# Kernel optimization log

Hardware: AMD Instinct MI355X
Metric: run time of the kernel (lower is better)

## Reference

```python
import jax, jax.numpy as jnp
import numpy as np

H, T, E = 8, 2048, 512


def setup_inputs() -> dict:
    key = jax.random.key(0)
    ks = jax.random.split(key, 11)
    s_e = 1.0 / np.sqrt(E)
    s_f = 1.0 / np.sqrt(H * T)
    return {
        "x": jax.random.normal(ks[0], (T, E), jnp.float32),
        "y": jax.random.normal(ks[1], (T, E), jnp.float32),
        "z": jax.random.normal(ks[2], (T, E), jnp.float32),
        "Wq": jax.random.normal(ks[3], (H, E, E), jnp.float32) * s_e,
        "bq": jax.random.normal(ks[4], (H, E), jnp.float32) * s_e,
        "Wk": jax.random.normal(ks[5], (H, E, E), jnp.float32) * s_e,
        "bk": jax.random.normal(ks[6], (H, E), jnp.float32) * s_e,
        "Wv": jax.random.normal(ks[7], (H, E, E), jnp.float32) * s_e,
        "bv": jax.random.normal(ks[8], (H, E), jnp.float32) * s_e,
        "Wf": jax.random.normal(ks[9], (T, H * T), jnp.float32) * s_f,
        "bf": jax.random.normal(ks[10], (T,), jnp.float32) * s_f,
    }


def reference(x, y, z, Wq, bq, Wk, bk, Wv, bv, Wf, bf):
    # Per-head projections: torch Linear is x @ W.T + b, W is [out,in]
    q = jnp.einsum("se,hfe->hsf", x, Wq) + bq[:, None, :]  # [H,T,E]
    k = jnp.einsum("se,hfe->hsf", y, Wk) + bk[:, None, :]
    v = jnp.einsum("se,hfe->hsf", z, Wv) + bv[:, None, :]
    # Scores scaled by sqrt(num query rows) = sqrt(T), as in the source
    scores = jnp.einsum("hsf,htf->hst", q, k) / jnp.sqrt(jnp.asarray(T, x.dtype))
    att = jax.nn.softmax(scores, axis=-1)
    heads_out = jnp.einsum("hst,htf->hsf", att, v)  # [H,T,E]
    concat = heads_out.reshape(H * T, E)  # cat along dim 0
    # finalLinear applied to concat.T: [E, H*T] @ Wf.T -> [E, T], then transpose
    final = (concat.T @ Wf.T + bf).T  # [T, E]
    residual = final + z
    # Manual per-row LayerNorm: (x - mean) / sqrt(std^2 + 1e-4), population std
    mean = jnp.mean(residual, axis=1, keepdims=True)
    var = jnp.var(residual, axis=1, keepdims=True)
    return (residual - mean) / jnp.sqrt(var + 1e-4)
```

## Files before the change

kernel.cpp:

```cpp
#include <hip/hip_runtime.h>
#include <hip/hip_bf16.h>
#include <cstdint>


#define HH 8
#define TT 2048
#define EE 512
#define HT (HH * TT)
#define HE (HH * EE)

typedef __bf16 bf16_t;
typedef __attribute__((ext_vector_type(8))) __bf16 bf16x8;
typedef __attribute__((ext_vector_type(4))) float f32x4;

__device__ __forceinline__ void gld_lds16(const bf16_t* __restrict__ g, bf16_t* l) {
  __builtin_amdgcn_global_load_lds(
      (const __attribute__((address_space(1))) unsigned int*)g,
      (__attribute__((address_space(3))) unsigned int*)l, 16, 0, 0);
}

__device__ __forceinline__ bf16x8 cvt8(float4 u, float4 v) {
  bf16x8 o;
  o[0] = (__bf16)u.x; o[1] = (__bf16)u.y; o[2] = (__bf16)u.z; o[3] = (__bf16)u.w;
  o[4] = (__bf16)v.x; o[5] = (__bf16)v.y; o[6] = (__bf16)v.z; o[7] = (__bf16)v.w;
  return o;
}

template <typename AT, typename CT>
__global__ __launch_bounds__(512, 4) void mfma_gemm_nt(
    const AT* __restrict__ A, const bf16_t* __restrict__ B, CT* __restrict__ C,
    const float* __restrict__ bias_m, const float* __restrict__ bias_n,
    int K, int lda, int ldb, int ldc,
    int64_t sA, int64_t sB, int64_t sC, int64_t sBM, int64_t sBN) {
  const int gx = gridDim.x, gy = gridDim.y;
  const int nwg = gx * gy * (int)gridDim.z;
  const int lin = blockIdx.x + gx * (blockIdx.y + gy * blockIdx.z);
  const int qn = nwg >> 3, rn = nwg & 7;
  const int xcd = lin & 7, sub = lin >> 3;
  const int wgid = (xcd < rn ? xcd * (qn + 1) : rn * (qn + 1) + (xcd - rn) * qn) + sub;
  const int bx = wgid % gx;
  const int t1 = wgid / gx;
  const int by = t1 % gy;
  const int z = t1 / gy;

  A += z * sA;
  B += z * sB;
  C += z * sC;
  if (bias_m) bias_m += z * sBM;
  if (bias_n) bias_n += z * sBN;

  const int m0 = bx * 128;
  const int n0 = by * 128;
  const int tid = threadIdx.x;

  __shared__ bf16_t sAb[2][128 * 64];
  __shared__ bf16_t sBb[2][128 * 64];

  const int srow = tid >> 3;
  const int sc = tid & 7;
  const int csw = (sc ^ (srow & 7)) * 8;
  const AT* a0 = A + (int64_t)(m0 + srow) * lda + csw;
  const AT* a1 = a0 + (int64_t)64 * lda;
  const bf16_t* b0 = B + (int64_t)(n0 + srow) * ldb + csw;
  const bf16_t* b1 = b0 + (int64_t)64 * ldb;

  const int wave = tid >> 6;
  const int lane = tid & 63;
  const int wm = (wave >> 2) * 64;
  const int wn = (wave & 3) * 32;
  const int fr = lane & 15;
  const int qd = lane >> 4;
  const int cx0 = ((0 * 4 + qd) ^ (fr & 7)) * 8;
  const int cx1 = ((1 * 4 + qd) ^ (fr & 7)) * 8;

  f32x4 acc[4][2];
#pragma unroll
  for (int i = 0; i < 4; i++)
#pragma unroll
    for (int j = 0; j < 2; j++) acc[i][j] = (f32x4){0.f, 0.f, 0.f, 0.f};

  float4 pa[4];

#define STAGE_B(buf, kt)                                   \
  do {                                                     \
    gld_lds16(b0 + (kt), &sBb[buf][tid * 8]);              \
    gld_lds16(b1 + (kt), &sBb[buf][4096 + tid * 8]);       \
  } while (0)

#define STAGE_A_BF16(buf, kt)                              \
  do {                                                     \
    gld_lds16(a0 + (kt), &sAb[buf][tid * 8]);              \
    gld_lds16(a1 + (kt), &sAb[buf][4096 + tid * 8]);       \
  } while (0)

#define LOAD_A_F32(kt)                                     \
  do {                                                     \
    pa[0] = ((const float4*)(a0 + (kt)))[0];               \
    pa[1] = ((const float4*)(a0 + (kt)))[1];               \
    pa[2] = ((const float4*)(a1 + (kt)))[0];               \
    pa[3] = ((const float4*)(a1 + (kt)))[1];               \
  } while (0)

#define WRITE_A_F32(buf)                                      \
  do {                                                        \
    *(bf16x8*)&sAb[buf][tid * 8] = cvt8(pa[0], pa[1]);        \
    *(bf16x8*)&sAb[buf][4096 + tid * 8] = cvt8(pa[2], pa[3]); \
  } while (0)

#define COMPUTE(buf)                                                                    \
  do {                                                                                  \
    bf16x8 af[2][4], bfr[2][2];                                                         \
    _Pragma("unroll") for (int i = 0; i < 4; i++) {                                     \
      const int ar = (wm + i * 16 + fr) * 64;                                           \
      af[0][i] = *(const bf16x8*)&sAb[buf][ar + cx0];                                   \
      af[1][i] = *(const bf16x8*)&sAb[buf][ar + cx1];                                   \
    }                                                                                   \
    _Pragma("unroll") for (int j = 0; j < 2; j++) {                                     \
      const int br = (wn + j * 16 + fr) * 64;                                           \
      bfr[0][j] = *(const bf16x8*)&sBb[buf][br + cx0];                                  \
      bfr[1][j] = *(const bf16x8*)&sBb[buf][br + cx1];                                  \
    }                                                                                   \
    _Pragma("unroll") for (int ks = 0; ks < 2; ks++)                                    \
        _Pragma("unroll") for (int i = 0; i < 4; i++)                                   \
            _Pragma("unroll") for (int j = 0; j < 2; j++)                               \
                acc[i][j] = __builtin_amdgcn_mfma_f32_16x16x32_bf16(                    \
                    af[ks][i], bfr[ks][j], acc[i][j], 0, 0, 0);                         \
  } while (0)

  if constexpr (sizeof(AT) == 2) {
    STAGE_A_BF16(0, 0);
  } else {
    LOAD_A_F32(0);
    WRITE_A_F32(0);
  }
  STAGE_B(0, 0);
  __syncthreads();

  for (int kt = 0; kt < K; kt += 128) {
    if constexpr (sizeof(AT) == 2) {
      STAGE_A_BF16(1, kt + 64);
    } else {
      LOAD_A_F32(kt + 64);
    }
    STAGE_B(1, kt + 64);
    COMPUTE(0);
    if constexpr (sizeof(AT) == 4) WRITE_A_F32(1);
    __syncthreads();

    const bool more = (kt + 128) < K;
    if (more) {
      if constexpr (sizeof(AT) == 2) {
        STAGE_A_BF16(0, kt + 128);
      } else {
        LOAD_A_F32(kt + 128);
      }
      STAGE_B(0, kt + 128);
    }
    COMPUTE(1);
    if constexpr (sizeof(AT) == 4) {
      if (more) WRITE_A_F32(0);
    }
    __syncthreads();
  }

#undef STAGE_B
#undef STAGE_A_BF16
#undef LOAD_A_F32
#undef WRITE_A_F32
#undef COMPUTE

#pragma unroll
  for (int i = 0; i < 4; i++) {
    const int row0 = m0 + wm + i * 16 + qd * 4;
#pragma unroll
    for (int j = 0; j < 2; j++) {
      const int col = n0 + wn + j * 16 + fr;
      const float bn = bias_n ? bias_n[col] : 0.f;
#pragma unroll
      for (int r = 0; r < 4; r++) {
        const float bm = bias_m ? bias_m[row0 + r] : 0.f;
        C[(int64_t)(row0 + r) * ldc + col] = (CT)(acc[i][j][r] + bn + bm);
      }
    }
  }
}

__global__ __launch_bounds__(256) void cvt_bf16(const float* __restrict__ s,
                                                bf16_t* __restrict__ d) {
  const int64_t i = ((int64_t)blockIdx.x * 256 + threadIdx.x) * 8;
  float4 u = ((const float4*)(s + i))[0];
  float4 v = ((const float4*)(s + i))[1];
  *(bf16x8*)(d + i) = cvt8(u, v);
}

__global__ __launch_bounds__(256) void softmax_rows(bf16_t* __restrict__ S) {
  const float scale = 0.022097086912079608f;
  bf16_t* p = S + (int64_t)blockIdx.x * TT;
  const int tid = threadIdx.x;
  bf16x8 in = *(const bf16x8*)(p + tid * 8);
  float v[8];
  float mx = -1e30f;
#pragma unroll
  for (int i = 0; i < 8; i++) {
    v[i] = (float)in[i] * scale;
    mx = fmaxf(mx, v[i]);
  }
#pragma unroll
  for (int o = 32; o > 0; o >>= 1) mx = fmaxf(mx, __shfl_xor(mx, o));
  __shared__ float redm[4], reds[4];
  if ((tid & 63) == 0) redm[tid >> 6] = mx;
  __syncthreads();
  mx = fmaxf(fmaxf(redm[0], redm[1]), fmaxf(redm[2], redm[3]));
  float sum = 0.f;
#pragma unroll
  for (int i = 0; i < 8; i++) {
    v[i] = __expf(v[i] - mx);
    sum += v[i];
  }
#pragma unroll
  for (int o = 32; o > 0; o >>= 1) sum += __shfl_xor(sum, o);
  if ((tid & 63) == 0) reds[tid >> 6] = sum;
  __syncthreads();
  sum = reds[0] + reds[1] + reds[2] + reds[3];
  const float inv = 1.0f / sum;
  bf16x8 o8;
#pragma unroll
  for (int i = 0; i < 8; i++) o8[i] = (__bf16)(v[i] * inv);
  *(bf16x8*)(p + tid * 8) = o8;
}

__global__ __launch_bounds__(256) void ln_res(const float* __restrict__ F,
                                              const float* __restrict__ Z,
                                              const float* __restrict__ BF,
                                              float* __restrict__ O, int np) {
  const int row = blockIdx.x;
  const int tid = threadIdx.x;
  const int64_t off = (int64_t)row * EE + tid;
  float a = 0.f, b = 0.f;
  for (int pz = 0; pz < np; pz++) {
    const float* f = F + (int64_t)pz * TT * EE;
    a += f[off];
    b += f[off + 256];
  }
  const float bft = BF[row];
  a += bft + Z[off];
  b += bft + Z[off + 256];
  float s = a + b, ss = a * a + b * b;
#pragma unroll
  for (int w = 32; w > 0; w >>= 1) {
    s += __shfl_xor(s, w);
    ss += __shfl_xor(ss, w);
  }
  __shared__ float rs[4], rss[4];
  if ((tid & 63) == 0) {
    rs[tid >> 6] = s;
    rss[tid >> 6] = ss;
  }
  __syncthreads();
  s = rs[0] + rs[1] + rs[2] + rs[3];
  ss = rss[0] + rss[1] + rss[2] + rss[3];
  const float mean = s * (1.0f / EE);
  const float var = ss * (1.0f / EE) - mean * mean;
  const float inv = rsqrtf(var + 1e-4f);
  float* o = O + (int64_t)row * EE;
  o[tid] = (a - mean) * inv;
  o[tid + 256] = (b - mean) * inv;
}

extern "C" void kernel_launch(void* const* d_in, const int* in_sizes, int n_in,
                              void* d_out, int out_size, void* d_ws, size_t ws_size,
                              hipStream_t stream) {
  const float* x = (const float*)d_in[0];
  const float* y = (const float*)d_in[1];
  const float* z = (const float*)d_in[2];
  const float* Wq = (const float*)d_in[3];
  const float* bq = (const float*)d_in[4];
  const float* Wk = (const float*)d_in[5];
  const float* bk = (const float*)d_in[6];
  const float* Wv = (const float*)d_in[7];
  const float* bv = (const float*)d_in[8];
  const float* Wf = (const float*)d_in[9];
  const float* bfb = (const float*)d_in[10];
  float* out = (float*)d_out;

  const size_t MB = 1ull << 20;
  char* p = (char*)d_ws;

  const int64_t nTE = (int64_t)TT * EE;
  const int64_t nW = (int64_t)HH * EE * EE;

  if (ws_size >= 151 * MB) {
    bf16_t* xb = (bf16_t*)(p + 0 * MB);
    bf16_t* yb = (bf16_t*)(p + 2 * MB);
    bf16_t* zb = (bf16_t*)(p + 4 * MB);
    bf16_t* Wqb = (bf16_t*)(p + 6 * MB);
    bf16_t* Wkb = (bf16_t*)(p + 10 * MB);
    bf16_t* Wvb = (bf16_t*)(p + 14 * MB);
    bf16_t* q = (bf16_t*)(p + 18 * MB);
    bf16_t* k = (bf16_t*)(p + 34 * MB);
    bf16_t* vT = (bf16_t*)(p + 50 * MB);
    bf16_t* att = (bf16_t*)(p + 66 * MB);
    bf16_t* hoT = (bf16_t*)(p + 130 * MB);
    float* finp = (float*)(p + 66 * MB);

    cvt_bf16<<<nTE / 2048, 256, 0, stream>>>(x, xb);
    cvt_bf16<<<nTE / 2048, 256, 0, stream>>>(y, yb);
    cvt_bf16<<<nTE / 2048, 256, 0, stream>>>(z, zb);
    cvt_bf16<<<nW / 2048, 256, 0, stream>>>(Wq, Wqb);
    cvt_bf16<<<nW / 2048, 256, 0, stream>>>(Wk, Wkb);
    cvt_bf16<<<nW / 2048, 256, 0, stream>>>(Wv, Wvb);

    mfma_gemm_nt<bf16_t, bf16_t><<<dim3(16, 32, 1), 512, 0, stream>>>(
        xb, Wqb, q, nullptr, bq, EE, EE, EE, HE, 0, 0, 0, 0, 0);
    mfma_gemm_nt<bf16_t, bf16_t><<<dim3(16, 32, 1), 512, 0, stream>>>(
        yb, Wkb, k, nullptr, bk, EE, EE, EE, HE, 0, 0, 0, 0, 0);
    mfma_gemm_nt<bf16_t, bf16_t><<<dim3(32, 16, 1), 512, 0, stream>>>(
        Wvb, zb, vT, bv, nullptr, EE, EE, EE, TT, 0, 0, 0, 0, 0);
    mfma_gemm_nt<bf16_t, bf16_t><<<dim3(16, 16, 8), 512, 0, stream>>>(
        q, k, att, nullptr, nullptr, EE, HE, HE, TT, EE, EE, (int64_t)TT * TT, 0, 0);
    softmax_rows<<<HH * TT, 256, 0, stream>>>(att);
    mfma_gemm_nt<bf16_t, bf16_t><<<dim3(4, 16, 8), 512, 0, stream>>>(
        vT, att, hoT, nullptr, nullptr, TT, TT, TT, HT, (int64_t)EE * TT, (int64_t)TT * TT,
        (int64_t)TT, 0, 0);
    mfma_gemm_nt<float, float><<<dim3(16, 4, 8), 512, 0, stream>>>(
        Wf, hoT, finp, nullptr, nullptr, HT / 8, HT, HT, EE, HT / 8, HT / 8,
        (int64_t)TT * EE, 0, 0);
    ln_res<<<TT, 256, 0, stream>>>(finp, z, bfb, out, 8);
  } else {
    bf16_t* xb = (bf16_t*)(p + 0 * MB);
    bf16_t* yb = (bf16_t*)(p + 2 * MB);
    bf16_t* zb = (bf16_t*)(p + 4 * MB);
    bf16_t* Wqb = (bf16_t*)(p + 6 * MB);
    bf16_t* Wkb = (bf16_t*)(p + 10 * MB);
    bf16_t* Wvb = (bf16_t*)(p + 14 * MB);
    bf16_t* qh = (bf16_t*)(p + 18 * MB);
    bf16_t* kh = (bf16_t*)(p + 20 * MB);
    bf16_t* vTh = (bf16_t*)(p + 22 * MB);
    bf16_t* att = (bf16_t*)(p + 24 * MB);
    bf16_t* hoT = (bf16_t*)(p + 32 * MB);
    float* finp = (float*)(p + 0 * MB);

    cvt_bf16<<<nTE / 2048, 256, 0, stream>>>(x, xb);
    cvt_bf16<<<nTE / 2048, 256, 0, stream>>>(y, yb);
    cvt_bf16<<<nTE / 2048, 256, 0, stream>>>(z, zb);
    cvt_bf16<<<nW / 2048, 256, 0, stream>>>(Wq, Wqb);
    cvt_bf16<<<nW / 2048, 256, 0, stream>>>(Wk, Wkb);
    cvt_bf16<<<nW / 2048, 256, 0, stream>>>(Wv, Wvb);

    for (int h = 0; h < HH; h++) {
      const bf16_t* Wq_h = Wqb + (int64_t)h * EE * EE;
      const bf16_t* Wk_h = Wkb + (int64_t)h * EE * EE;
      const bf16_t* Wv_h = Wvb + (int64_t)h * EE * EE;
      mfma_gemm_nt<bf16_t, bf16_t><<<dim3(16, 4, 1), 512, 0, stream>>>(
          xb, Wq_h, qh, nullptr, bq + h * EE, EE, EE, EE, EE, 0, 0, 0, 0, 0);
      mfma_gemm_nt<bf16_t, bf16_t><<<dim3(16, 4, 1), 512, 0, stream>>>(
          yb, Wk_h, kh, nullptr, bk + h * EE, EE, EE, EE, EE, 0, 0, 0, 0, 0);
      mfma_gemm_nt<bf16_t, bf16_t><<<dim3(4, 16, 1), 512, 0, stream>>>(
          Wv_h, zb, vTh, bv + h * EE, nullptr, EE, EE, EE, TT, 0, 0, 0, 0, 0);
      mfma_gemm_nt<bf16_t, bf16_t><<<dim3(16, 16, 1), 512, 0, stream>>>(
          qh, kh, att, nullptr, nullptr, EE, EE, EE, TT, 0, 0, 0, 0, 0);
      softmax_rows<<<TT, 256, 0, stream>>>(att);
      mfma_gemm_nt<bf16_t, bf16_t><<<dim3(4, 16, 1), 512, 0, stream>>>(
          vTh, att, hoT + (int64_t)h * TT, nullptr, nullptr, TT, TT, TT, HT, 0, 0, 0, 0, 0);
    }
    mfma_gemm_nt<float, float><<<dim3(16, 4, 8), 512, 0, stream>>>(
        Wf, hoT, finp, nullptr, nullptr, HT / 8, HT, HT, EE, HT / 8, HT / 8,
        (int64_t)TT * EE, 0, 0);
    ln_res<<<TT, 256, 0, stream>>>(finp, z, bfb, out, 8);
  }
}
```

Baseline: 430.5 us.

## Add 256x256-tile 8-phase pipelined bf16 GEMM for QK projections and scores

Adds a new GEMM kernel with 256x256 output tiles per 512-thread block and 128KB of LDS. Its software pipeline interleaves direct global-to-LDS loads, LDS fragment reads and MFMA quadrants with explicit waitcnt, barriers and setprio. It is used for the attention score GEMM, and for the Q and K projections, which are merged into one batched launch by relying on the contiguous workspace layout plus a device copy of the two bias vectors. Larger tiles raise data reuse per LDS load and cut launch count, but the grids become much smaller (256 and 512 blocks) and the kernel can hold fewer waves per CU.

```diff
diff --git a/kernel.cpp b/kernel.cpp
--- a/kernel.cpp
+++ b/kernel.cpp
@@ -24,6 +24,171 @@
   o[0] = (__bf16)u.x; o[1] = (__bf16)u.y; o[2] = (__bf16)u.z; o[3] = (__bf16)u.w;
   o[4] = (__bf16)v.x; o[5] = (__bf16)v.y; o[6] = (__bf16)v.z; o[7] = (__bf16)v.w;
   return o;
+}
+
+#define XCD_SWIZZLE()                                                              \
+  const int gx = gridDim.x, gy = gridDim.y;                                        \
+  const int nwg = gx * gy * (int)gridDim.z;                                        \
+  const int lin = blockIdx.x + gx * (blockIdx.y + gy * blockIdx.z);                \
+  const int qn_ = nwg >> 3, rn_ = nwg & 7;                                         \
+  const int xcd_ = lin & 7, sub_ = lin >> 3;                                       \
+  const int wgid =                                                                 \
+      (xcd_ < rn_ ? xcd_ * (qn_ + 1) : rn_ * (qn_ + 1) + (xcd_ - rn_) * qn_) + sub_; \
+  const int bx = wgid % gx;                                                        \
+  const int t1_ = wgid / gx;                                                       \
+  const int by = t1_ % gy;                                                         \
+  const int z = t1_ / gy;
+
+template <typename CT>
+__global__ __launch_bounds__(512, 2) void gemm256_8ph(
+    const bf16_t* __restrict__ A, const bf16_t* __restrict__ B, CT* __restrict__ C,
+    const float* __restrict__ bias_n,
+    int K, int lda, int ldb, int ldc,
+    int64_t sA, int64_t sB, int64_t sC, int64_t sBN) {
+  XCD_SWIZZLE();
+  A += z * sA;
+  B += z * sB;
+  C += z * sC;
+  if (bias_n) bias_n += z * sBN;
+
+  const int m0 = bx * 256;
+  const int n0 = by * 256;
+  const int tid = threadIdx.x;
+
+  __shared__ bf16_t lds[65536];
+  bf16_t* sAl = lds;
+  bf16_t* sBl = lds + 32768;
+
+  const int srow = tid >> 3;
+  const int csw = ((tid & 7) ^ (srow & 7)) * 8;
+  const bf16_t* aS = A + (int64_t)(m0 + srow) * lda + csw;
+  const bf16_t* bS = B + (int64_t)(n0 + srow) * ldb + csw;
+  const int64_t l64a = (int64_t)64 * lda, l64b = (int64_t)64 * ldb;
+
+  const int wave = tid >> 6, lane = tid & 63;
+  const int wr = wave >> 2, wc = wave & 3;
+  const int fr = lane & 15, qd = lane >> 4;
+  const int aoff = wr * 8192 + fr * 64;
+  const int boff = wc * 4096 + fr * 64;
+  const int ck0 = ((0 * 4 + qd) ^ (fr & 7)) * 8;
+  const int ck1 = ((1 * 4 + qd) ^ (fr & 7)) * 8;
+
+  f32x4 acc[8][4];
+#pragma unroll
+  for (int i = 0; i < 8; i++)
+#pragma unroll
+    for (int j = 0; j < 4; j++) acc[i][j] = (f32x4){0.f, 0.f, 0.f, 0.f};
+
+  bf16x8 aR[2][8];
+  bf16x8 bR[2][2];
+
+#define STG_A(d, h, t)                                                        \
+  do {                                                                        \
+    const bf16_t* g_ = aS + (int64_t)(h) * 128 * lda + (int64_t)(t) * 64;     \
+    gld_lds16(g_, &sAl[(d) * 16384 + (h) * 8192 + tid * 8]);                  \
+    gld_lds16(g_ + l64a, &sAl[(d) * 16384 + (h) * 8192 + 4096 + tid * 8]);    \
+  } while (0)
+#define STG_B(d, h, t)                                                        \
+  do {                                                                        \
+    const bf16_t* g_ = bS + (int64_t)(h) * 128 * ldb + (int64_t)(t) * 64;     \
+    gld_lds16(g_, &sBl[(d) * 16384 + (h) * 8192 + tid * 8]);                  \
+    gld_lds16(g_ + l64b, &sBl[(d) * 16384 + (h) * 8192 + 4096 + tid * 8]);    \
+  } while (0)
+#define RD_A(d, ih)                                                           \
+  _Pragma("unroll") for (int i_ = 0; i_ < 4; i_++) {                          \
+    const int b_ = (d) * 16384 + aoff + ((ih) * 4 + i_) * 1024;               \
+    aR[0][(ih) * 4 + i_] = *(const bf16x8*)&sAl[b_ + ck0];                    \
+    aR[1][(ih) * 4 + i_] = *(const bf16x8*)&sAl[b_ + ck1];                    \
+  }
+#define RD_B(d, jh)                                                           \
+  _Pragma("unroll") for (int j_ = 0; j_ < 2; j_++) {                          \
+    const int b_ = (d) * 16384 + boff + ((jh) * 2 + j_) * 1024;               \
+    bR[0][j_] = *(const bf16x8*)&sBl[b_ + ck0];                               \
+    bR[1][j_] = *(const bf16x8*)&sBl[b_ + ck1];                               \
+  }
+#define MM(qm, qn)                                                            \
+  do {                                                                        \
+    __builtin_amdgcn_s_setprio(1);                                            \
+    _Pragma("unroll") for (int ks = 0; ks < 2; ks++)                          \
+        _Pragma("unroll") for (int i_ = 0; i_ < 4; i_++)                      \
+            _Pragma("unroll") for (int j_ = 0; j_ < 2; j_++)                  \
+                acc[(qm) * 4 + i_][(qn) * 2 + j_] =                           \
+                    __builtin_amdgcn_mfma_f32_16x16x32_bf16(                  \
+                        aR[ks][(qm) * 4 + i_], bR[ks][j_],                    \
+                        acc[(qm) * 4 + i_][(qn) * 2 + j_], 0, 0, 0);          \
+    __builtin_amdgcn_s_setprio(0);                                            \
+  } while (0)
+#define BAR __builtin_amdgcn_s_barrier()
+#define LGKM0                                                                 \
+  do {                                                                        \
+    asm volatile("s_waitcnt lgkmcnt(0)" ::: "memory");                        \
+    __builtin_amdgcn_sched_barrier(0);                                        \
+  } while (0)
+#define VMC(n)                                                                \
+  do {                                                                        \
+    asm volatile("s_waitcnt vmcnt(" #n ")" ::: "memory");                     \
+    __builtin_amdgcn_sched_barrier(0);                                        \
+  } while (0)
+
+  const int NT = K >> 6;
+
+  STG_A(0, 0, 0); STG_A(0, 1, 0); STG_B(0, 0, 0); STG_B(0, 1, 0);
+  STG_A(1, 0, 1); STG_A(1, 1, 1);
+  VMC(4);
+  BAR;
+
+  for (int t0 = 0; t0 < NT; t0 += 2) {
+    const int t1 = t0 + 1;
+    const bool m2 = (t0 + 2) < NT;
+    RD_A(0, 0); RD_B(0, 0);
+    STG_B(1, 0, t1);
+    BAR; LGKM0; MM(0, 0); BAR;
+    RD_A(0, 1);
+    STG_B(1, 1, t1);
+    BAR; LGKM0; MM(1, 0); BAR;
+    RD_B(0, 1);
+    if (m2) STG_A(0, 0, t0 + 2);
+    BAR; LGKM0; MM(0, 1); BAR;
+    if (m2) STG_A(0, 1, t0 + 2);
+    BAR; MM(1, 1);
+    if (m2) { VMC(4); } else { VMC(0); }
+    BAR;
+    RD_A(1, 0); RD_B(1, 0);
+    if (m2) STG_B(0, 0, t0 + 2);
+    BAR; LGKM0; MM(0, 0); BAR;
+    RD_A(1, 1);
+    if (m2) STG_B(0, 1, t0 + 2);
+    BAR; LGKM0; MM(1, 0); BAR;
+    RD_B(1, 1);
+    if (m2) STG_A(1, 0, t1 + 2);
+    BAR; LGKM0; MM(0, 1); BAR;
+    if (m2) STG_A(1, 1, t1 + 2);
+    BAR; MM(1, 1);
+    if (m2) VMC(4);
+    BAR;
+  }
+
+#undef STG_A
+#undef STG_B
+#undef RD_A
+#undef RD_B
+#undef MM
+#undef BAR
+#undef LGKM0
+#undef VMC
+
+#pragma unroll
+  for (int i = 0; i < 8; i++) {
+    const int row0 = m0 + wr * 128 + i * 16 + qd * 4;
+#pragma unroll
+    for (int j = 0; j < 4; j++) {
+      const int col = n0 + wc * 64 + j * 16 + fr;
+      const float bn = bias_n ? bias_n[col] : 0.f;
+#pragma unroll
+      for (int r = 0; r < 4; r++)
+        C[(int64_t)(row0 + r) * ldc + col] = (CT)(acc[i][j][r] + bn);
+    }
+  }
 }
 
 template <typename AT, typename CT>
@@ -32,17 +197,7 @@
     const float* __restrict__ bias_m, const float* __restrict__ bias_n,
     int K, int lda, int ldb, int ldc,
     int64_t sA, int64_t sB, int64_t sC, int64_t sBM, int64_t sBN) {
-  const int gx = gridDim.x, gy = gridDim.y;
-  const int nwg = gx * gy * (int)gridDim.z;
-  const int lin = blockIdx.x + gx * (blockIdx.y + gy * blockIdx.z);
-  const int qn = nwg >> 3, rn = nwg & 7;
-  const int xcd = lin & 7, sub = lin >> 3;
-  const int wgid = (xcd < rn ? xcd * (qn + 1) : rn * (qn + 1) + (xcd - rn) * qn) + sub;
-  const int bx = wgid % gx;
-  const int t1 = wgid / gx;
-  const int by = t1 % gy;
-  const int z = t1 / gy;
-
+  XCD_SWIZZLE();
   A += z * sA;
   B += z * sB;
   C += z * sC;
@@ -81,50 +236,46 @@
 
   float4 pa[4];
 
-#define STAGE_B(buf, kt)                                   \
-  do {                                                     \
-    gld_lds16(b0 + (kt), &sBb[buf][tid * 8]);              \
-    gld_lds16(b1 + (kt), &sBb[buf][4096 + tid * 8]);       \
-  } while (0)
-
-#define STAGE_A_BF16(buf, kt)                              \
-  do {                                                     \
-    gld_lds16(a0 + (kt), &sAb[buf][tid * 8]);              \
-    gld_lds16(a1 + (kt), &sAb[buf][4096 + tid * 8]);       \
-  } while (0)
-
-#define LOAD_A_F32(kt)                                     \
-  do {                                                     \
-    pa[0] = ((const float4*)(a0 + (kt)))[0];               \
-    pa[1] = ((const float4*)(a0 + (kt)))[1];               \
-    pa[2] = ((const float4*)(a1 + (kt)))[0];               \
-    pa[3] = ((const float4*)(a1 + (kt)))[1];               \
-  } while (0)
-
+#define STAGE_B(buf, kt)                              \
+  do {                                                \
+    gld_lds16(b0 + (kt), &sBb[buf][tid * 8]);         \
+    gld_lds16(b1 + (kt), &sBb[buf][4096 + tid * 8]);  \
+  } while (0)
+#define STAGE_A_BF16(buf, kt)                         \
+  do {                                                \
+    gld_lds16(a0 + (kt), &sAb[buf][tid * 8]);         \
+    gld_lds16(a1 + (kt), &sAb[buf][4096 + tid * 8]);  \
+  } while (0)
+#define LOAD_A_F32(kt)                                \
+  do {                                                \
+    pa[0] = ((const float4*)(a0 + (kt)))[0];          \
+    pa[1] = ((const float4*)(a0 + (kt)))[1];          \
+    pa[2] = ((const float4*)(a1 + (kt)))[0];          \
+    pa[3] = ((const float4*)(a1 + (kt)))[1];          \
+  } while (0)
 #define WRITE_A_F32(buf)                                      \
   do {                                                        \
     *(bf16x8*)&sAb[buf][tid * 8] = cvt8(pa[0], pa[1]);        \
     *(bf16x8*)&sAb[buf][4096 + tid * 8] = cvt8(pa[2], pa[3]); \
   } while (0)
-
-#define COMPUTE(buf)                                                                    \
-  do {                                                                                  \
-    bf16x8 af[2][4], bfr[2][2];                                                         \
-    _Pragma("unroll") for (int i = 0; i < 4; i++) {                                     \
-      const int ar = (wm + i * 16 + fr) * 64;                                           \
-      af[0][i] = *(const bf16x8*)&sAb[buf][ar + cx0];                                   \
-      af[1][i] = *(const bf16x8*)&sAb[buf][ar + cx1];                                   \
-    }                                                                                   \
-    _Pragma("unroll") for (int j = 0; j < 2; j++) {                                     \
-      const int br = (wn + j * 16 + fr) * 64;                                           \
-      bfr[0][j] = *(const bf16x8*)&sBb[buf][br + cx0];                                  \
-      bfr[1][j] = *(const bf16x8*)&sBb[buf][br + cx1];                                  \
-    }                                                                                   \
-    _Pragma("unroll") for (int ks = 0; ks < 2; ks++)                                    \
-        _Pragma("unroll") for (int i = 0; i < 4; i++)                                   \
-            _Pragma("unroll") for (int j = 0; j < 2; j++)                               \
-                acc[i][j] = __builtin_amdgcn_mfma_f32_16x16x32_bf16(                    \
-                    af[ks][i], bfr[ks][j], acc[i][j], 0, 0, 0);                         \
+#define COMPUTE(buf)                                                                   \
+  do {                                                                                 \
+    bf16x8 af[2][4], bfr[2][2];                                                        \
+    _Pragma("unroll") for (int i = 0; i < 4; i++) {                                    \
+      const int ar = (wm + i * 16 + fr) * 64;                                          \
+      af[0][i] = *(const bf16x8*)&sAb[buf][ar + cx0];                                  \
+      af[1][i] = *(const bf16x8*)&sAb[buf][ar + cx1];                                  \
+    }                                                                                  \
+    _Pragma("unroll") for (int j = 0; j < 2; j++) {                                    \
+      const int br = (wn + j * 16 + fr) * 64;                                          \
+      bfr[0][j] = *(const bf16x8*)&sBb[buf][br + cx0];                                 \
+      bfr[1][j] = *(const bf16x8*)&sBb[buf][br + cx1];                                 \
+    }                                                                                  \
+    _Pragma("unroll") for (int ks = 0; ks < 2; ks++)                                   \
+        _Pragma("unroll") for (int i = 0; i < 4; i++)                                  \
+            _Pragma("unroll") for (int j = 0; j < 2; j++)                              \
+                acc[i][j] = __builtin_amdgcn_mfma_f32_16x16x32_bf16(                   \
+                    af[ks][i], bfr[ks][j], acc[i][j], 0, 0, 0);                        \
   } while (0)
 
   if constexpr (sizeof(AT) == 2) {
@@ -302,6 +453,7 @@
     bf16_t* att = (bf16_t*)(p + 66 * MB);
     bf16_t* hoT = (bf16_t*)(p + 130 * MB);
     float* finp = (float*)(p + 66 * MB);
+    float* bqk = (float*)(p + 146 * MB);
 
     cvt_bf16<<<nTE / 2048, 256, 0, stream>>>(x, xb);
     cvt_bf16<<<nTE / 2048, 256, 0, stream>>>(y, yb);
@@ -309,15 +461,16 @@
     cvt_bf16<<<nW / 2048, 256, 0, stream>>>(Wq, Wqb);
     cvt_bf16<<<nW / 2048, 256, 0, stream>>>(Wk, Wkb);
     cvt_bf16<<<nW / 2048, 256, 0, stream>>>(Wv, Wvb);
-
-    mfma_gemm_nt<bf16_t, bf16_t><<<dim3(16, 32, 1), 512, 0, stream>>>(
-        xb, Wqb, q, nullptr, bq, EE, EE, EE, HE, 0, 0, 0, 0, 0);
-    mfma_gemm_nt<bf16_t, bf16_t><<<dim3(16, 32, 1), 512, 0, stream>>>(
-        yb, Wkb, k, nullptr, bk, EE, EE, EE, HE, 0, 0, 0, 0, 0);
+    hipMemcpyAsync(bqk, bq, HE * sizeof(float), hipMemcpyDeviceToDevice, stream);
+    hipMemcpyAsync(bqk + HE, bk, HE * sizeof(float), hipMemcpyDeviceToDevice, stream);
+
+    gemm256_8ph<bf16_t><<<dim3(8, 16, 2), 512, 0, stream>>>(
+        xb, Wqb, q, bqk, EE, EE, EE, HE,
+        (int64_t)TT * EE, (int64_t)HE * EE, (int64_t)TT * HE, HE);
     mfma_gemm_nt<bf16_t, bf16_t><<<dim3(32, 16, 1), 512, 0, stream>>>(
         Wvb, zb, vT, bv, nullptr, EE, EE, EE, TT, 0, 0, 0, 0, 0);
-    mfma_gemm_nt<bf16_t, bf16_t><<<dim3(16, 16, 8), 512, 0, stream>>>(
-        q, k, att, nullptr, nullptr, EE, HE, HE, TT, EE, EE, (int64_t)TT * TT, 0, 0);
+    gemm256_8ph<bf16_t><<<dim3(8, 8, 8), 512, 0, stream>>>(
+        q, k, att, nullptr, EE, HE, HE, TT, EE, EE, (int64_t)TT * TT, 0);
     softmax_rows<<<HH * TT, 256, 0, stream>>>(att);
     mfma_gemm_nt<bf16_t, bf16_t><<<dim3(4, 16, 8), 512, 0, stream>>>(
         vT, att, hoT, nullptr, nullptr, TT, TT, TT, HT, (int64_t)EE * TT, (int64_t)TT * TT,
```

After: 428.8 us. Within noise of the previous version (-0.4%).
